# Optimization experiments

Hardware: AMD Instinct MI355X
Metric: run time of the kernel (lower is better)

The kernel has to match this reference:

```python
import jax, jax.numpy as jnp
import numpy as np

N_NODES = 10000
N_EDGES = 320000
NODE_DIM = 24
EDGE_DIM = 2
HID = 64


def setup_inputs() -> dict:
    key = jax.random.key(0)
    ks = jax.random.split(key, 12)
    s = 0.1  # param scale
    return {
        "x": jax.random.normal(ks[0], (N_NODES, NODE_DIM), dtype=jnp.float32),
        "edge_attr": jax.random.normal(ks[1], (N_EDGES, EDGE_DIM), dtype=jnp.float32),
        "edge_index": jax.random.randint(ks[2], (2, N_EDGES), 0, N_NODES, dtype=jnp.int64),
        "W_in": jax.random.normal(ks[3], (NODE_DIM, HID), dtype=jnp.float32) * s,
        "b_in": jnp.zeros((HID,), dtype=jnp.float32),
        "W_e": jax.random.normal(ks[4], (EDGE_DIM, HID), dtype=jnp.float32) * s,
        "b_e": jnp.zeros((HID,), dtype=jnp.float32),
        "W1": jax.random.normal(ks[5], (HID, HID), dtype=jnp.float32) * s,
        "b1": jnp.zeros((HID,), dtype=jnp.float32),
        "W2": jax.random.normal(ks[6], (HID, HID), dtype=jnp.float32) * s,
        "b2": jnp.zeros((HID,), dtype=jnp.float32),
        "M": jax.random.normal(ks[7], (HID, HID), dtype=jnp.float32) * s,
    }


def reference(x, edge_attr, W_in, b_in, W_e, b_e, W1, b1, W2, b2, M, edge_index):
    n = x.shape[0]
    src, dst = edge_index[0], edge_index[1]  # messages flow src -> dst (PyG convention)

    h = x @ W_in + b_in                      # [N, H]
    ea = edge_attr @ W_e + b_e               # [E, H]

    def gine(h):
        # GINEConv, eps=0: mlp(h_i + sum_j relu(h_j + e_ji)); both convs SHARE the mlp params
        msg = jax.nn.relu(h[src] + ea)                           # [E, H] gather
        agg = jax.ops.segment_sum(msg, dst, num_segments=n)      # [N, H] scatter-add
        z = h + agg
        return jax.nn.relu(z @ W1 + b1) @ W2 + b2

    h = jax.nn.relu(gine(h))
    h = gine(h)

    logits = (h @ M) @ h.T                   # [N, N] bilinear decode
    return jax.nn.softmax(logits, axis=1)
```

## Files before the change

### kernel.cpp

```cpp
#include <hip/hip_runtime.h>

typedef _Float16 half8 __attribute__((ext_vector_type(8)));
typedef float floatx4 __attribute__((ext_vector_type(4)));

#define N_NODES 10000
#define N_EDGES 320000
#define NODE_DIM 24
#define HID 64
#define KSPLIT 192
#define NPAD 10112
#define NT 625
#define NSEG 16
#define TPS 40
#define CSEG 25

__global__ __launch_bounds__(256) void k_embed_hist(
    const float* __restrict__ x, const float* __restrict__ Win,
    const float* __restrict__ bin, float* __restrict__ h0,
    const int* __restrict__ dst, int* __restrict__ cnt) {
  int t = blockIdx.x * blockDim.x + threadIdx.x;
  if (t < N_EDGES) atomicAdd(&cnt[dst[t]], 1);
  int n = t >> 6, j = t & 63;
  if (n >= N_NODES) return;
  float acc = bin[j];
  const float* xr = x + n * NODE_DIM;
#pragma unroll
  for (int k = 0; k < NODE_DIM; ++k) acc = fmaf(xr[k], Win[k * HID + j], acc);
  h0[n * HID + j] = acc;
}

__global__ __launch_bounds__(1024) void k_scan(const int* __restrict__ cnt,
                                               int* __restrict__ offs, int* __restrict__ cur) {
  __shared__ int part[1024];
  int tid = threadIdx.x;
  const int PER = 10;
  int base = tid * PER;
  int loc[PER];
  int s = 0;
#pragma unroll
  for (int i = 0; i < PER; ++i) {
    int e = base + i;
    int v = (e < N_NODES) ? cnt[e] : 0;
    loc[i] = s; s += v;
  }
  part[tid] = s;
  __syncthreads();
  for (int off = 1; off < 1024; off <<= 1) {
    int v = (tid >= off) ? part[tid - off] : 0;
    __syncthreads();
    part[tid] += v;
    __syncthreads();
  }
  int pre = (tid > 0) ? part[tid - 1] : 0;
#pragma unroll
  for (int i = 0; i < PER; ++i) {
    int e = base + i;
    if (e < N_NODES) { int o = pre + loc[i]; offs[e] = o; cur[e] = o; }
  }
  if (tid == 1023) offs[N_NODES] = pre + s;
}

__global__ __launch_bounds__(256) void k_scatter(const int* __restrict__ dst,
                                                 int* __restrict__ cur, int* __restrict__ csr) {
  int e = blockIdx.x * blockDim.x + threadIdx.x;
  if (e < N_EDGES) { int p = atomicAdd(&cur[dst[e]], 1); csr[p] = e; }
}

__global__ __launch_bounds__(256) void k_agg(
    const float* __restrict__ h, const float* __restrict__ eattr,
    const int* __restrict__ src, const int* __restrict__ csr, const int* __restrict__ offs,
    const float* __restrict__ We, const float* __restrict__ be, float* __restrict__ agg) {
  int t = blockIdx.x * blockDim.x + threadIdx.x;
  int n = t >> 6, j = t & 63;
  if (n >= N_NODES) return;
  float w0 = We[j], w1 = We[HID + j], b = be[j];
  const float2* ea2 = (const float2*)eattr;
  float acc = 0.f;
  int e0 = offs[n], e1 = offs[n + 1];
  int i = e0;
  for (; i + 1 < e1; i += 2) {
    int ea_ = csr[i], eb_ = csr[i + 1];
    int sa = src[ea_], sb = src[eb_];
    float2 aa = ea2[ea_], ab = ea2[eb_];
    float va = h[sa * HID + j] + fmaf(aa.x, w0, fmaf(aa.y, w1, b));
    float vb = h[sb * HID + j] + fmaf(ab.x, w0, fmaf(ab.y, w1, b));
    acc += fmaxf(va, 0.f) + fmaxf(vb, 0.f);
  }
  if (i < e1) {
    int ea_ = csr[i];
    int sa = src[ea_];
    float2 aa = ea2[ea_];
    float va = h[sa * HID + j] + fmaf(aa.x, w0, fmaf(aa.y, w1, b));
    acc += fmaxf(va, 0.f);
  }
  agg[n * HID + j] = acc;
}

__global__ __launch_bounds__(256) void k_mlp(
    const float* __restrict__ h, const float* __restrict__ agg,
    const float* __restrict__ W1, const float* __restrict__ b1,
    const float* __restrict__ W2, const float* __restrict__ b2,
    float* __restrict__ hout, int dorelu) {
  __shared__ float zs[4][HID];
  __shared__ float ts[4][HID];
  int t = blockIdx.x * blockDim.x + threadIdx.x;
  int n = t >> 6, j = t & 63, nl = threadIdx.x >> 6;
  float z = h[n * HID + j] + agg[n * HID + j];
  zs[nl][j] = z;
  __syncthreads();
  float acc = b1[j];
#pragma unroll 16
  for (int k = 0; k < HID; ++k) acc = fmaf(zs[nl][k], W1[k * HID + j], acc);
  float tv = fmaxf(acc, 0.f);
  ts[nl][j] = tv;
  __syncthreads();
  float acc2 = b2[j];
#pragma unroll 16
  for (int k = 0; k < HID; ++k) acc2 = fmaf(ts[nl][k], W2[k * HID + j], acc2);
  hout[n * HID + j] = dorelu ? fmaxf(acc2, 0.f) : acc2;
}

__global__ __launch_bounds__(256) void k_mlp2_prep(
    const float* __restrict__ h, const float* __restrict__ agg,
    const float* __restrict__ W1, const float* __restrict__ b1,
    const float* __restrict__ W2, const float* __restrict__ b2,
    const float* __restrict__ Mw, _Float16* __restrict__ Ap, _Float16* __restrict__ Bf) {
  __shared__ float zs[4][HID];
  __shared__ float ts[4][HID];
  __shared__ float hs[4][HID];
  int t = blockIdx.x * blockDim.x + threadIdx.x;
  int n = t >> 6, j = t & 63, nl = threadIdx.x >> 6;
  float z = h[n * HID + j] + agg[n * HID + j];
  zs[nl][j] = z;
  __syncthreads();
  float acc = b1[j];
#pragma unroll 16
  for (int k = 0; k < HID; ++k) acc = fmaf(zs[nl][k], W1[k * HID + j], acc);
  float tv = fmaxf(acc, 0.f);
  ts[nl][j] = tv;
  __syncthreads();
  float acc2 = b2[j];
#pragma unroll 16
  for (int k = 0; k < HID; ++k) acc2 = fmaf(ts[nl][k], W2[k * HID + j], acc2);
  hs[nl][j] = acc2;
  {
    _Float16 bhi = (_Float16)acc2;
    _Float16 blo = (_Float16)(acc2 - (float)bhi);
    int ct = n >> 4, l16 = n & 15;
    int kk[3] = { j, 64 + j, 128 + j };
    _Float16 vv[3] = { bhi, blo, bhi };
#pragma unroll
    for (int q = 0; q < 3; ++q) {
      int k = kk[q];
      int s = k >> 5, quad = (k & 31) >> 3, jj = k & 7;
      Bf[((((ct * 6 + s) * 64) + quad * 16 + l16) << 3) + jj] = vv[q];
    }
  }
  __syncthreads();
  float accm = 0.f;
#pragma unroll 16
  for (int k = 0; k < HID; ++k) accm = fmaf(hs[nl][k], Mw[k * HID + j], accm);
  _Float16 ahi = (_Float16)accm;
  _Float16 alo = (_Float16)(accm - (float)ahi);
  _Float16* arow = Ap + (size_t)n * KSPLIT;
  arow[j] = ahi; arow[64 + j] = ahi; arow[128 + j] = alo;
}

__global__ __launch_bounds__(256) void k_pass1(
    const _Float16* __restrict__ Ap, const _Float16* __restrict__ Bfh,
    float* __restrict__ pm, float* __restrict__ ps) {
  int seg = blockIdx.x & 15;
  int rg = blockIdx.x >> 4;
  int wave = threadIdx.x >> 6, lane = threadIdx.x & 63;
  int quad = lane >> 4, l16 = lane & 15;
  int rowbase = rg * 128 + wave * 32;
  const half8* A = (const half8*)Ap;
  const half8* Bf = (const half8*)Bfh;
  half8 af[2][6];
#pragma unroll
  for (int tt = 0; tt < 2; ++tt) {
    int ar = rowbase + tt * 16 + l16;
#pragma unroll
    for (int s = 0; s < 6; ++s) af[tt][s] = A[ar * 24 + s * 4 + quad];
  }
  float m[8], sum[8];
#pragma unroll
  for (int i = 0; i < 8; ++i) { m[i] = -3.0e38f; sum[i] = 0.f; }
  int ct0 = seg * TPS;
  int ct1 = ct0 + TPS; if (ct1 > NT) ct1 = NT;
  for (int ct = ct0; ct < ct1; ++ct) {
    half8 bf[6];
#pragma unroll
    for (int s = 0; s < 6; ++s) bf[s] = Bf[(ct * 6 + s) * 64 + lane];
    floatx4 acc0 = {0.f, 0.f, 0.f, 0.f}, acc1 = {0.f, 0.f, 0.f, 0.f};
#pragma unroll
    for (int s = 0; s < 6; ++s) {
      acc0 = __builtin_amdgcn_mfma_f32_16x16x32_f16(af[0][s], bf[s], acc0, 0, 0, 0);
      acc1 = __builtin_amdgcn_mfma_f32_16x16x32_f16(af[1][s], bf[s], acc1, 0, 0, 0);
    }
    float d[8];
#pragma unroll
    for (int i = 0; i < 4; ++i) { d[i] = acc0[i]; d[4 + i] = acc1[i]; }
    bool need = false;
#pragma unroll
    for (int i = 0; i < 8; ++i) need |= (d[i] > m[i] - 20.f);
    if (__any((int)need)) {
#pragma unroll
      for (int i = 0; i < 8; ++i) {
        float nm = fmaxf(m[i], d[i]);
        sum[i] = sum[i] * __expf(m[i] - nm) + __expf(d[i] - nm);
        m[i] = nm;
      }
    }
  }
#pragma unroll
  for (int off = 1; off < 16; off <<= 1) {
#pragma unroll
    for (int i = 0; i < 8; ++i) {
      float mo = __shfl_xor(m[i], off);
      float so = __shfl_xor(sum[i], off);
      float nm = fmaxf(m[i], mo);
      sum[i] = sum[i] * __expf(m[i] - nm) + so * __expf(mo - nm);
      m[i] = nm;
    }
  }
  if (l16 == 0) {
#pragma unroll
    for (int i = 0; i < 8; ++i) {
      int row = rowbase + (i >> 2) * 16 + quad * 4 + (i & 3);
      if (row < N_NODES) {
        pm[seg * N_NODES + row] = m[i];
        ps[seg * N_NODES + row] = sum[i];
      }
    }
  }
}

__global__ __launch_bounds__(256) void k_combine(
    const float* __restrict__ pm, const float* __restrict__ ps,
    float* __restrict__ Mrow, float* __restrict__ iS) {
  int r = blockIdx.x * blockDim.x + threadIdx.x;
  if (r >= N_NODES) return;
  float M = -3.0e38f;
#pragma unroll
  for (int s = 0; s < NSEG; ++s) M = fmaxf(M, pm[s * N_NODES + r]);
  float S = 0.f;
#pragma unroll
  for (int s = 0; s < NSEG; ++s) S += ps[s * N_NODES + r] * __expf(pm[s * N_NODES + r] - M);
  Mrow[r] = M;
  iS[r] = 1.f / S;
}

__global__ __launch_bounds__(256) void k_pass2(
    const _Float16* __restrict__ Ap, const _Float16* __restrict__ Bfh,
    const float* __restrict__ Mrow, const float* __restrict__ iS, float* __restrict__ out) {
  int cs = blockIdx.x % CSEG;
  int rg = blockIdx.x / CSEG;
  int wave = threadIdx.x >> 6, lane = threadIdx.x & 63;
  int quad = lane >> 4, l16 = lane & 15;
  int rowbase = rg * 128 + wave * 32;
  const half8* A = (const half8*)Ap;
  const half8* Bf = (const half8*)Bfh;
  half8 af[2][6];
#pragma unroll
  for (int tt = 0; tt < 2; ++tt) {
    int ar = rowbase + tt * 16 + l16;
#pragma unroll
    for (int s = 0; s < 6; ++s) af[tt][s] = A[ar * 24 + s * 4 + quad];
  }
  float Mv[8], Iv[8];
  int rowv[8];
#pragma unroll
  for (int i = 0; i < 8; ++i) {
    int row = rowbase + (i >> 2) * 16 + quad * 4 + (i & 3);
    rowv[i] = row;
    Mv[i] = (row < N_NODES) ? Mrow[row] : 0.f;
    Iv[i] = (row < N_NODES) ? iS[row] : 0.f;
  }
  for (int ct = cs * CSEG; ct < cs * CSEG + CSEG; ++ct) {
    half8 bf[6];
#pragma unroll
    for (int s = 0; s < 6; ++s) bf[s] = Bf[(ct * 6 + s) * 64 + lane];
    floatx4 acc0 = {0.f, 0.f, 0.f, 0.f}, acc1 = {0.f, 0.f, 0.f, 0.f};
#pragma unroll
    for (int s = 0; s < 6; ++s) {
      acc0 = __builtin_amdgcn_mfma_f32_16x16x32_f16(af[0][s], bf[s], acc0, 0, 0, 0);
      acc1 = __builtin_amdgcn_mfma_f32_16x16x32_f16(af[1][s], bf[s], acc1, 0, 0, 0);
    }
    float d[8];
#pragma unroll
    for (int i = 0; i < 4; ++i) { d[i] = acc0[i]; d[4 + i] = acc1[i]; }
    int col = ct * 16 + l16;
#pragma unroll
    for (int i = 0; i < 8; ++i) {
      if (rowv[i] < N_NODES) {
        float v = __expf(d[i] - Mv[i]) * Iv[i];
        __builtin_nontemporal_store(v, &out[(size_t)rowv[i] * N_NODES + col]);
      }
    }
  }
}

extern "C" void kernel_launch(void* const* d_in, const int* in_sizes, int n_in,
                              void* d_out, int out_size, void* d_ws, size_t ws_size,
                              hipStream_t stream) {
  const float* x     = (const float*)d_in[0];
  const float* eattr = (const float*)d_in[1];
  const int*   eidx  = (const int*)d_in[2];
  const float* Win   = (const float*)d_in[3];
  const float* bin   = (const float*)d_in[4];
  const float* We    = (const float*)d_in[5];
  const float* be    = (const float*)d_in[6];
  const float* W1    = (const float*)d_in[7];
  const float* b1    = (const float*)d_in[8];
  const float* W2    = (const float*)d_in[9];
  const float* b2    = (const float*)d_in[10];
  const float* Mw    = (const float*)d_in[11];
  float* out = (float*)d_out;
  const int* src = eidx;
  const int* dst = eidx + N_EDGES;

  char* w = (char*)d_ws;
  auto alloc = [&](size_t bytes) { char* p = w; w += (bytes + 255) & ~(size_t)255; return p; };
  float*    h0   = (float*)alloc((size_t)N_NODES * HID * 4);
  float*    agg  = (float*)alloc((size_t)N_NODES * HID * 4);
  float*    h1   = (float*)alloc((size_t)N_NODES * HID * 4);
  _Float16* Ap   = (_Float16*)alloc((size_t)NPAD * KSPLIT * 2);
  _Float16* Bf   = (_Float16*)alloc((size_t)NT * 6 * 64 * 8 * 2);
  int*      csr  = (int*)alloc((size_t)N_EDGES * 4);
  int*      cnt  = (int*)alloc((size_t)(N_NODES + 1) * 4);
  int*      offs = (int*)alloc((size_t)(N_NODES + 1) * 4);
  int*      cur  = (int*)alloc((size_t)(N_NODES + 1) * 4);
  float*    pm   = (float*)alloc((size_t)NSEG * N_NODES * 4);
  float*    ps   = (float*)alloc((size_t)NSEG * N_NODES * 4);
  float*    Mrow = (float*)alloc((size_t)N_NODES * 4);
  float*    iS   = (float*)alloc((size_t)N_NODES * 4);

  hipMemsetAsync(cnt, 0, (N_NODES + 1) * 4, stream);
  hipMemsetAsync(Ap + (size_t)N_NODES * KSPLIT, 0, (size_t)(NPAD - N_NODES) * KSPLIT * 2, stream);

  k_embed_hist<<<(N_NODES * HID) / 256, 256, 0, stream>>>(x, Win, bin, h0, dst, cnt);
  k_scan<<<1, 1024, 0, stream>>>(cnt, offs, cur);
  k_scatter<<<N_EDGES / 256, 256, 0, stream>>>(dst, cur, csr);

  k_agg<<<(N_NODES * HID) / 256, 256, 0, stream>>>(h0, eattr, src, csr, offs, We, be, agg);
  k_mlp<<<(N_NODES * HID) / 256, 256, 0, stream>>>(h0, agg, W1, b1, W2, b2, h1, 1);
  k_agg<<<(N_NODES * HID) / 256, 256, 0, stream>>>(h1, eattr, src, csr, offs, We, be, agg);
  k_mlp2_prep<<<(N_NODES * HID) / 256, 256, 0, stream>>>(h1, agg, W1, b1, W2, b2, Mw, Ap, Bf);

  k_pass1<<<79 * NSEG, 256, 0, stream>>>(Ap, Bf, pm, ps);
  k_combine<<<(N_NODES + 255) / 256, 256, 0, stream>>>(pm, ps, Mrow, iS);
  k_pass2<<<79 * CSEG, 256, 0, stream>>>(Ap, Bf, Mrow, iS, out);
}
```

Measured before the change: 748.2 us.

## Fuse aggregation into MLP kernels, fold combine into pass2, simplify softmax stats

Merges each neighbour-aggregation kernel with the following GINE MLP kernel, so the agg buffer is never written to or read back from global memory. The row max/sum combine step moves into the prologue of pass2, which removes a launch and the Mrow/iS arrays. The padding memset is replaced by zeroing inside block 0 of the second GINE kernel. Pass1's online softmax now uses the first tile as a fixed reference and skips rescaling unless a value exceeds it by 8, trading exactness of the running max for fewer exponentials. It also drops the node bounds check in k_gine1, which is safe only because the grid covers exactly N_NODES.

```diff
diff --git a/kernel.cpp b/kernel.cpp
--- a/kernel.cpp
+++ b/kernel.cpp
@@ -66,13 +66,17 @@
   if (e < N_EDGES) { int p = atomicAdd(&cur[dst[e]], 1); csr[p] = e; }
 }
 
-__global__ __launch_bounds__(256) void k_agg(
+__global__ __launch_bounds__(256) void k_gine1(
     const float* __restrict__ h, const float* __restrict__ eattr,
     const int* __restrict__ src, const int* __restrict__ csr, const int* __restrict__ offs,
-    const float* __restrict__ We, const float* __restrict__ be, float* __restrict__ agg) {
+    const float* __restrict__ We, const float* __restrict__ be,
+    const float* __restrict__ W1, const float* __restrict__ b1,
+    const float* __restrict__ W2, const float* __restrict__ b2,
+    float* __restrict__ hout) {
+  __shared__ float zs[4][HID];
+  __shared__ float ts[4][HID];
   int t = blockIdx.x * blockDim.x + threadIdx.x;
-  int n = t >> 6, j = t & 63;
-  if (n >= N_NODES) return;
+  int n = t >> 6, j = t & 63, nl = threadIdx.x >> 6;
   float w0 = We[j], w1 = We[HID + j], b = be[j];
   const float2* ea2 = (const float2*)eattr;
   float acc = 0.f;
@@ -93,59 +97,73 @@
     float va = h[sa * HID + j] + fmaf(aa.x, w0, fmaf(aa.y, w1, b));
     acc += fmaxf(va, 0.f);
   }
-  agg[n * HID + j] = acc;
-}
-
-__global__ __launch_bounds__(256) void k_mlp(
-    const float* __restrict__ h, const float* __restrict__ agg,
-    const float* __restrict__ W1, const float* __restrict__ b1,
-    const float* __restrict__ W2, const float* __restrict__ b2,
-    float* __restrict__ hout, int dorelu) {
-  __shared__ float zs[4][HID];
-  __shared__ float ts[4][HID];
-  int t = blockIdx.x * blockDim.x + threadIdx.x;
-  int n = t >> 6, j = t & 63, nl = threadIdx.x >> 6;
-  float z = h[n * HID + j] + agg[n * HID + j];
+  float z = h[n * HID + j] + acc;
   zs[nl][j] = z;
   __syncthreads();
-  float acc = b1[j];
-#pragma unroll 16
-  for (int k = 0; k < HID; ++k) acc = fmaf(zs[nl][k], W1[k * HID + j], acc);
-  float tv = fmaxf(acc, 0.f);
+  float a1 = b1[j];
+#pragma unroll 16
+  for (int k = 0; k < HID; ++k) a1 = fmaf(zs[nl][k], W1[k * HID + j], a1);
+  float tv = fmaxf(a1, 0.f);
   ts[nl][j] = tv;
   __syncthreads();
-  float acc2 = b2[j];
-#pragma unroll 16
-  for (int k = 0; k < HID; ++k) acc2 = fmaf(ts[nl][k], W2[k * HID + j], acc2);
-  hout[n * HID + j] = dorelu ? fmaxf(acc2, 0.f) : acc2;
-}
-
-__global__ __launch_bounds__(256) void k_mlp2_prep(
-    const float* __restrict__ h, const float* __restrict__ agg,
+  float a2 = b2[j];
+#pragma unroll 16
+  for (int k = 0; k < HID; ++k) a2 = fmaf(ts[nl][k], W2[k * HID + j], a2);
+  hout[n * HID + j] = fmaxf(a2, 0.f);
+}
+
+__global__ __launch_bounds__(256) void k_gine2_prep(
+    const float* __restrict__ h, const float* __restrict__ eattr,
+    const int* __restrict__ src, const int* __restrict__ csr, const int* __restrict__ offs,
+    const float* __restrict__ We, const float* __restrict__ be,
     const float* __restrict__ W1, const float* __restrict__ b1,
     const float* __restrict__ W2, const float* __restrict__ b2,
     const float* __restrict__ Mw, _Float16* __restrict__ Ap, _Float16* __restrict__ Bf) {
   __shared__ float zs[4][HID];
   __shared__ float ts[4][HID];
   __shared__ float hs[4][HID];
+  if (blockIdx.x == 0) {
+    unsigned int* pad = (unsigned int*)(Ap + (size_t)N_NODES * KSPLIT);
+    for (int idx = threadIdx.x; idx < (NPAD - N_NODES) * KSPLIT / 2; idx += 256) pad[idx] = 0u;
+  }
   int t = blockIdx.x * blockDim.x + threadIdx.x;
   int n = t >> 6, j = t & 63, nl = threadIdx.x >> 6;
-  float z = h[n * HID + j] + agg[n * HID + j];
+  float w0 = We[j], w1 = We[HID + j], b = be[j];
+  const float2* ea2 = (const float2*)eattr;
+  float acc = 0.f;
+  int e0 = offs[n], e1 = offs[n + 1];
+  int i = e0;
+  for (; i + 1 < e1; i += 2) {
+    int ea_ = csr[i], eb_ = csr[i + 1];
+    int sa = src[ea_], sb = src[eb_];
+    float2 aa = ea2[ea_], ab = ea2[eb_];
+    float va = h[sa * HID + j] + fmaf(aa.x, w0, fmaf(aa.y, w1, b));
+    float vb = h[sb * HID + j] + fmaf(ab.x, w0, fmaf(ab.y, w1, b));
+    acc += fmaxf(va, 0.f) + fmaxf(vb, 0.f);
+  }
+  if (i < e1) {
+    int ea_ = csr[i];
+    int sa = src[ea_];
+    float2 aa = ea2[ea_];
+    float va = h[sa * HID + j] + fmaf(aa.x, w0, fmaf(aa.y, w1, b));
+    acc += fmaxf(va, 0.f);
+  }
+  float z = h[n * HID + j] + acc;
   zs[nl][j] = z;
   __syncthreads();
-  float acc = b1[j];
-#pragma unroll 16
-  for (int k = 0; k < HID; ++k) acc = fmaf(zs[nl][k], W1[k * HID + j], acc);
-  float tv = fmaxf(acc, 0.f);
+  float a1 = b1[j];
+#pragma unroll 16
+  for (int k = 0; k < HID; ++k) a1 = fmaf(zs[nl][k], W1[k * HID + j], a1);
+  float tv = fmaxf(a1, 0.f);
   ts[nl][j] = tv;
   __syncthreads();
-  float acc2 = b2[j];
-#pragma unroll 16
-  for (int k = 0; k < HID; ++k) acc2 = fmaf(ts[nl][k], W2[k * HID + j], acc2);
-  hs[nl][j] = acc2;
+  float a2 = b2[j];
+#pragma unroll 16
+  for (int k = 0; k < HID; ++k) a2 = fmaf(ts[nl][k], W2[k * HID + j], a2);
+  hs[nl][j] = a2;
   {
-    _Float16 bhi = (_Float16)acc2;
-    _Float16 blo = (_Float16)(acc2 - (float)bhi);
+    _Float16 bhi = (_Float16)a2;
+    _Float16 blo = (_Float16)(a2 - (float)bhi);
     int ct = n >> 4, l16 = n & 15;
     int kk[3] = { j, 64 + j, 128 + j };
     _Float16 vv[3] = { bhi, blo, bhi };
@@ -183,11 +201,10 @@
 #pragma unroll
     for (int s = 0; s < 6; ++s) af[tt][s] = A[ar * 24 + s * 4 + quad];
   }
-  float m[8], sum[8];
-#pragma unroll
-  for (int i = 0; i < 8; ++i) { m[i] = -3.0e38f; sum[i] = 0.f; }
+  float f[8], sm[8];
   int ct0 = seg * TPS;
   int ct1 = ct0 + TPS; if (ct1 > NT) ct1 = NT;
+  bool first = true;
   for (int ct = ct0; ct < ct1; ++ct) {
     half8 bf[6];
 #pragma unroll
@@ -201,15 +218,24 @@
     float d[8];
 #pragma unroll
     for (int i = 0; i < 4; ++i) { d[i] = acc0[i]; d[4 + i] = acc1[i]; }
-    bool need = false;
-#pragma unroll
-    for (int i = 0; i < 8; ++i) need |= (d[i] > m[i] - 20.f);
-    if (__any((int)need)) {
-#pragma unroll
-      for (int i = 0; i < 8; ++i) {
-        float nm = fmaxf(m[i], d[i]);
-        sum[i] = sum[i] * __expf(m[i] - nm) + __expf(d[i] - nm);
-        m[i] = nm;
+    if (first) {
+      first = false;
+#pragma unroll
+      for (int i = 0; i < 8; ++i) { f[i] = d[i]; sm[i] = 1.f; }
+    } else {
+      bool resc = false;
+#pragma unroll
+      for (int i = 0; i < 8; ++i) resc |= (d[i] > f[i] + 8.f);
+      if (__any((int)resc)) {
+#pragma unroll
+        for (int i = 0; i < 8; ++i) {
+          float nf = fmaxf(f[i], d[i]);
+          sm[i] = sm[i] * __expf(f[i] - nf) + __expf(d[i] - nf);
+          f[i] = nf;
+        }
+      } else {
+#pragma unroll
+        for (int i = 0; i < 8; ++i) sm[i] += __expf(d[i] - f[i]);
       }
     }
   }
@@ -217,11 +243,11 @@
   for (int off = 1; off < 16; off <<= 1) {
 #pragma unroll
     for (int i = 0; i < 8; ++i) {
-      float mo = __shfl_xor(m[i], off);
-      float so = __shfl_xor(sum[i], off);
-      float nm = fmaxf(m[i], mo);
-      sum[i] = sum[i] * __expf(m[i] - nm) + so * __expf(mo - nm);
-      m[i] = nm;
+      float fo = __shfl_xor(f[i], off);
+      float so = __shfl_xor(sm[i], off);
+      float nf = fmaxf(f[i], fo);
+      sm[i] = sm[i] * __expf(f[i] - nf) + so * __expf(fo - nf);
+      f[i] = nf;
     }
   }
   if (l16 == 0) {
@@ -229,33 +255,31 @@
     for (int i = 0; i < 8; ++i) {
       int row = rowbase + (i >> 2) * 16 + quad * 4 + (i & 3);
       if (row < N_NODES) {
-        pm[seg * N_NODES + row] = m[i];
-        ps[seg * N_NODES + row] = sum[i];
+        pm[seg * N_NODES + row] = f[i];
+        ps[seg * N_NODES + row] = sm[i];
       }
     }
   }
-}
-
-__global__ __launch_bounds__(256) void k_combine(
-    const float* __restrict__ pm, const float* __restrict__ ps,
-    float* __restrict__ Mrow, float* __restrict__ iS) {
-  int r = blockIdx.x * blockDim.x + threadIdx.x;
-  if (r >= N_NODES) return;
-  float M = -3.0e38f;
-#pragma unroll
-  for (int s = 0; s < NSEG; ++s) M = fmaxf(M, pm[s * N_NODES + r]);
-  float S = 0.f;
-#pragma unroll
-  for (int s = 0; s < NSEG; ++s) S += ps[s * N_NODES + r] * __expf(pm[s * N_NODES + r] - M);
-  Mrow[r] = M;
-  iS[r] = 1.f / S;
 }
 
 __global__ __launch_bounds__(256) void k_pass2(
     const _Float16* __restrict__ Ap, const _Float16* __restrict__ Bfh,
-    const float* __restrict__ Mrow, const float* __restrict__ iS, float* __restrict__ out) {
+    const float* __restrict__ pm, const float* __restrict__ ps, float* __restrict__ out) {
+  __shared__ float Ms[128], Is[128];
   int cs = blockIdx.x % CSEG;
   int rg = blockIdx.x / CSEG;
+  for (int r = threadIdx.x; r < 128; r += 256) {
+    int row = rg * 128 + r;
+    if (row < N_NODES) {
+      float M = -3.0e38f;
+#pragma unroll
+      for (int s = 0; s < NSEG; ++s) M = fmaxf(M, pm[s * N_NODES + row]);
+      float S = 0.f;
+#pragma unroll
+      for (int s = 0; s < NSEG; ++s) S += ps[s * N_NODES + row] * __expf(pm[s * N_NODES + row] - M);
+      Ms[r] = M; Is[r] = 1.f / S;
+    } else { Ms[r] = 0.f; Is[r] = 0.f; }
+  }
   int wave = threadIdx.x >> 6, lane = threadIdx.x & 63;
   int quad = lane >> 4, l16 = lane & 15;
   int rowbase = rg * 128 + wave * 32;
@@ -268,14 +292,15 @@
 #pragma unroll
     for (int s = 0; s < 6; ++s) af[tt][s] = A[ar * 24 + s * 4 + quad];
   }
+  __syncthreads();
   float Mv[8], Iv[8];
   int rowv[8];
 #pragma unroll
   for (int i = 0; i < 8; ++i) {
-    int row = rowbase + (i >> 2) * 16 + quad * 4 + (i & 3);
-    rowv[i] = row;
-    Mv[i] = (row < N_NODES) ? Mrow[row] : 0.f;
-    Iv[i] = (row < N_NODES) ? iS[row] : 0.f;
+    int rl = wave * 32 + (i >> 2) * 16 + quad * 4 + (i & 3);
+    rowv[i] = rg * 128 + rl;
+    Mv[i] = Ms[rl];
+    Iv[i] = Is[rl];
   }
   for (int ct = cs * CSEG; ct < cs * CSEG + CSEG; ++ct) {
     half8 bf[6];
@@ -323,7 +348,6 @@
   char* w = (char*)d_ws;
   auto alloc = [&](size_t bytes) { char* p = w; w += (bytes + 255) & ~(size_t)255; return p; };
   float*    h0   = (float*)alloc((size_t)N_NODES * HID * 4);
-  float*    agg  = (float*)alloc((size_t)N_NODES * HID * 4);
   float*    h1   = (float*)alloc((size_t)N_NODES * HID * 4);
   _Float16* Ap   = (_Float16*)alloc((size_t)NPAD * KSPLIT * 2);
   _Float16* Bf   = (_Float16*)alloc((size_t)NT * 6 * 64 * 8 * 2);
@@ -333,22 +357,18 @@
   int*      cur  = (int*)alloc((size_t)(N_NODES + 1) * 4);
   float*    pm   = (float*)alloc((size_t)NSEG * N_NODES * 4);
   float*    ps   = (float*)alloc((size_t)NSEG * N_NODES * 4);
-  float*    Mrow = (float*)alloc((size_t)N_NODES * 4);
-  float*    iS   = (float*)alloc((size_t)N_NODES * 4);
 
   hipMemsetAsync(cnt, 0, (N_NODES + 1) * 4, stream);
-  hipMemsetAsync(Ap + (size_t)N_NODES * KSPLIT, 0, (size_t)(NPAD - N_NODES) * KSPLIT * 2, stream);
 
   k_embed_hist<<<(N_NODES * HID) / 256, 256, 0, stream>>>(x, Win, bin, h0, dst, cnt);
   k_scan<<<1, 1024, 0, stream>>>(cnt, offs, cur);
   k_scatter<<<N_EDGES / 256, 256, 0, stream>>>(dst, cur, csr);
 
-  k_agg<<<(N_NODES * HID) / 256, 256, 0, stream>>>(h0, eattr, src, csr, offs, We, be, agg);
-  k_mlp<<<(N_NODES * HID) / 256, 256, 0, stream>>>(h0, agg, W1, b1, W2, b2, h1, 1);
-  k_agg<<<(N_NODES * HID) / 256, 256, 0, stream>>>(h1, eattr, src, csr, offs, We, be, agg);
-  k_mlp2_prep<<<(N_NODES * HID) / 256, 256, 0, stream>>>(h1, agg, W1, b1, W2, b2, Mw, Ap, Bf);
+  k_gine1<<<(N_NODES * HID) / 256, 256, 0, stream>>>(
+      h0, eattr, src, csr, offs, We, be, W1, b1, W2, b2, h1);
+  k_gine2_prep<<<(N_NODES * HID) / 256, 256, 0, stream>>>(
+      h1, eattr, src, csr, offs, We, be, W1, b1, W2, b2, Mw, Ap, Bf);
 
   k_pass1<<<79 * NSEG, 256, 0, stream>>>(Ap, Bf, pm, ps);
-  k_combine<<<(N_NODES + 255) / 256, 256, 0, stream>>>(pm, ps, Mrow, iS);
-  k_pass2<<<79 * CSEG, 256, 0, stream>>>(Ap, Bf, Mrow, iS, out);
-}
+  k_pass2<<<79 * CSEG, 256, 0, stream>>>(Ap, Bf, pm, ps, out);
+}
```

Result: faster. 720.9 us (-3.6%).
